# Performance work log

Hardware: AMD Instinct MI355X
Metric: run time of the kernel (lower is better)

Reference implementation:

```python
import jax, jax.numpy as jnp
import numpy as np
from jax import lax

N_NODES = 19
N_FILT = 8
CONV_CH = N_NODES * N_FILT  # 152
T = 512
POOL = 4
T_POOL = T // POOL  # 128
GCN_OUT = 16
FLAT = N_NODES * GCN_OUT * T_POOL  # 38912
HID = 128
N_CLS = 2
BN_EPS = 1e-5


def setup_inputs() -> dict:
    key = jax.random.key(0)
    ks = jax.random.split(key, 12)
    B = 1024
    x = jax.random.normal(ks[0], (B, N_NODES, T), dtype=jnp.float32)
    # grouped Conv1d(19 -> 152, k=5, groups=19): kernel (out_ch, in_ch/groups=1, k)
    conv_w = jax.random.normal(ks[1], (CONV_CH, 1, 5), dtype=jnp.float32) * 0.2
    conv_b = jax.random.normal(ks[2], (CONV_CH,), dtype=jnp.float32) * 0.05
    bn_gamma = jnp.ones((CONV_CH,), jnp.float32)
    bn_beta = jnp.zeros((CONV_CH,), jnp.float32)
    bn_mean = jax.random.normal(ks[3], (CONV_CH,), dtype=jnp.float32) * 0.1
    bn_var = jax.random.uniform(ks[4], (CONV_CH,), dtype=jnp.float32, minval=0.5, maxval=1.5)
    adj = jax.random.uniform(ks[5], (N_NODES, N_NODES), dtype=jnp.float32)
    gcn_w = jax.random.normal(ks[6], (GCN_OUT, N_FILT), dtype=jnp.float32) * (1.0 / np.sqrt(N_FILT))
    gcn_b = jnp.zeros((GCN_OUT,), jnp.float32)
    w1 = jax.random.normal(ks[7], (HID, FLAT), dtype=jnp.float32) * (1.0 / np.sqrt(FLAT))
    b1 = jnp.zeros((HID,), jnp.float32)
    w2 = jax.random.normal(ks[8], (N_CLS, HID), dtype=jnp.float32) * (1.0 / np.sqrt(HID))
    b2 = jnp.zeros((N_CLS,), jnp.float32)
    return dict(x=x, conv_w=conv_w, conv_b=conv_b, bn_gamma=bn_gamma, bn_beta=bn_beta,
                bn_mean=bn_mean, bn_var=bn_var, adj=adj, gcn_w=gcn_w, gcn_b=gcn_b,
                w1=w1, b1=b1, w2=w2, b2=b2)


def reference(x, conv_w, conv_b, bn_gamma, bn_beta, bn_mean, bn_var, adj,
              gcn_w, gcn_b, w1, b1, w2, b2):
    B = x.shape[0]
    # depthwise temporal conv: [B,19,T] -> [B,152,T]
    h = lax.conv_general_dilated(x, conv_w, window_strides=(1,), padding=[(2, 2)],
                                 feature_group_count=N_NODES,
                                 dimension_numbers=('NCW', 'OIW', 'NCW'))
    h = h + conv_b[None, :, None]
    # BatchNorm1d (eval mode: running stats) + ReLU, fused elementwise
    inv = bn_gamma / jnp.sqrt(bn_var + BN_EPS)
    h = jax.nn.relu(h * inv[None, :, None] + (bn_beta - bn_mean * inv)[None, :, None])
    # MaxPool1d(4): [B,152,512] -> [B,152,128]
    h = h.reshape(B, CONV_CH, T_POOL, POOL).max(axis=-1)
    # view -> [B,19,8,128]
    h = h.reshape(B, N_NODES, N_FILT, T_POOL)
    # softmax adjacency aggregation: bift = A_ij * bjft
    A = jax.nn.softmax(adj, axis=1)
    support = jnp.einsum('ij,bjft->bift', A, h)
    # permute to [B,19,128,8], linear 8->16, ReLU
    g = jax.nn.relu(jnp.einsum('bnft,of->bnto', support, gcn_w) + gcn_b)
    # classifier: flatten -> Linear(38912,128) -> ReLU -> (Dropout eval=identity) -> Linear(128,2)
    flat = g.reshape(B, FLAT)
    hid = jax.nn.relu(flat @ w1.T + b1)
    return hid @ w2.T + b2
```

## Files before the change

### kernel.cpp

```cpp
#include <hip/hip_runtime.h>

#define NB    1024
#define NN    19
#define NF    8
#define CCH   152
#define TLEN  512
#define TP    128
#define GO    16
#define KFLAT 38912
#define HID   128
#define NCLS  2
#define NROWS (NB*TP)
#define KC    152
#define KP    160
#define NJP   20
#define NOUT  304
#define M2R   320

#define KTILE 1024
#define NKT   (KFLAT / KTILE)

typedef float  f32x4  __attribute__((ext_vector_type(4)));
typedef __bf16 bf16x8 __attribute__((ext_vector_type(8)));
typedef __bf16 bf16x4 __attribute__((ext_vector_type(4)));
typedef unsigned short u16x8 __attribute__((ext_vector_type(8)));

__device__ __forceinline__ void gload16(const __bf16* g, __bf16* l) {
    __builtin_amdgcn_global_load_lds(
        (const __attribute__((address_space(1))) void*)g,
        (__attribute__((address_space(3))) void*)l, 16, 0, 0);
}

__global__ __launch_bounds__(256) void prep_small(
    const float* __restrict__ adj,
    const float* __restrict__ bn_gamma, const float* __restrict__ bn_beta,
    const float* __restrict__ bn_mean,  const float* __restrict__ bn_var,
    const float* __restrict__ conv_b,
    float* __restrict__ A_g, float* __restrict__ bnS, float* __restrict__ bnB)
{
    const int tid = threadIdx.x;
    if (tid < NN) {
        float v[NN];
        float m = -1e30f;
        #pragma unroll
        for (int j = 0; j < NN; ++j) { v[j] = adj[tid * NN + j]; m = fmaxf(m, v[j]); }
        float s = 0.f;
        #pragma unroll
        for (int j = 0; j < NN; ++j) { v[j] = expf(v[j] - m); s += v[j]; }
        float rc = 1.f / s;
        #pragma unroll
        for (int j = 0; j < NN; ++j) A_g[tid * NN + j] = v[j] * rc;
    }
    if (tid >= 64 && tid < 64 + CCH) {
        int c = tid - 64;
        float inv = bn_gamma[c] * rsqrtf(bn_var[c] + 1e-5f);
        bnS[c] = inv;
        bnB[c] = conv_b[c] * inv + bn_beta[c] - bn_mean[c] * inv;
    }
}

__global__ __launch_bounds__(256) void prep_m2(
    const float* __restrict__ A_g, const float* __restrict__ gcn_w,
    __bf16* __restrict__ m2g)
{
    int i = blockIdx.x * 256 + threadIdx.x;
    if (i >= M2R * KP) return;
    int c = i / KP, k = i - c * KP;
    float v = 0.f;
    if (c < NOUT && k < KC) {
        int n = c >> 4, o = c & 15;
        int j = k >> 3, f = k & 7;
        v = A_g[n * NN + j] * gcn_w[o * NF + f];
    }
    m2g[i] = (__bf16)v;
}

__global__ __launch_bounds__(128) void conv_pool(
    const float* __restrict__ x,
    const float* __restrict__ conv_w,
    const float* __restrict__ bnS, const float* __restrict__ bnB,
    __bf16* __restrict__ H)
{
    const int bid = blockIdx.x;
    const int b = bid / NN, n = bid - b * NN;
    const int tp = threadIdx.x;

    const float* xr = x + ((size_t)b * NN + n) * TLEN;
    const float4 f4z = {0.f, 0.f, 0.f, 0.f};
    float4 L0 = (tp > 0)   ? *(const float4*)(xr + 4 * tp - 4) : f4z;
    float4 L1 =              *(const float4*)(xr + 4 * tp);
    float4 L2 = (tp < 127) ? *(const float4*)(xr + 4 * tp + 4) : f4z;
    float xv[9] = {L0.z, L0.w, L1.x, L1.y, L1.z, L1.w, L2.x, L2.y, L2.z};

    const float* cw = conv_w + n * (NF * 5);
    const float* Sp = bnS + n * NF;
    const float* Bp = bnB + n * NF;

    union { __bf16 h[8]; u16x8 v; } hv;
    #pragma unroll
    for (int f = 0; f < NF; ++f) {
        float w0 = cw[f*5+0], w1 = cw[f*5+1], w2 = cw[f*5+2], w3 = cw[f*5+3], w4 = cw[f*5+4];
        float s = Sp[f], bb = Bp[f];
        float m = -1e30f;
        #pragma unroll
        for (int p = 0; p < 4; ++p) {
            float a = xv[p]*w0 + xv[p+1]*w1 + xv[p+2]*w2 + xv[p+3]*w3 + xv[p+4]*w4;
            m = fmaxf(m, a * s + bb);
        }
        hv.h[f] = (__bf16)fmaxf(m, 0.f);
    }
    size_t row = (size_t)b * TP + tp;
    *(u16x8*)(H + ((size_t)n * NROWS + row) * 8) = hv.v;
    if (n == NN - 1) {
        u16x8 z = {0,0,0,0,0,0,0,0};
        *(u16x8*)(H + ((size_t)(NJP - 1) * NROWS + row) * 8) = z;
    }
}

__global__ __launch_bounds__(640) void mix_gcn(
    const __bf16* __restrict__ H,
    const __bf16* __restrict__ m2g,
    const float* __restrict__ gcn_b,
    __bf16* __restrict__ g2)
{
    const int tid  = threadIdx.x;
    const int lane = tid & 63, w = tid >> 6;
    const int arow = lane & 15;
    const int jg   = lane >> 4;
    const int ct0  = w * 2;

    const float4 gbv = *(const float4*)(gcn_b + jg * 4);

    bf16x8 mf[2][5];
    #pragma unroll
    for (int ct = 0; ct < 2; ++ct)
        #pragma unroll
        for (int ks = 0; ks < 5; ++ks)
            mf[ct][ks] = *(const bf16x8*)(
                m2g + (size_t)((ct0 + ct) * 16 + arow) * KP + ks * 32 + jg * 8);

    const int b = blockIdx.x;
    const __bf16* hbase = H + (size_t)arow * 8 + (size_t)jg * (NROWS * 8);

    bf16x8 afb[2][5];
    #pragma unroll
    for (int ks = 0; ks < 5; ++ks)
        afb[0][ks] = *(const bf16x8*)(hbase + ((size_t)b * TP) * 8 + (size_t)ks * 4 * (NROWS * 8));

    #pragma unroll
    for (int it = 0; it < 8; ++it) {
        if (it + 1 < 8) {
            #pragma unroll
            for (int ks = 0; ks < 5; ++ks)
                afb[(it + 1) & 1][ks] = *(const bf16x8*)(
                    hbase + ((size_t)b * TP + (it + 1) * 16) * 8 + (size_t)ks * 4 * (NROWS * 8));
        }

        f32x4 acc[2];
        #pragma unroll
        for (int ct = 0; ct < 2; ++ct) acc[ct] = (f32x4){0.f, 0.f, 0.f, 0.f};

        #pragma unroll
        for (int ks = 0; ks < 5; ++ks)
            #pragma unroll
            for (int ct = 0; ct < 2; ++ct)
                acc[ct] = __builtin_amdgcn_mfma_f32_16x16x32_bf16(mf[ct][ks], afb[it & 1][ks], acc[ct], 0, 0, 0);

        const int t = it * 16 + arow;
        __bf16* gb2 = g2 + (size_t)b * KFLAT + t * 16 + jg * 4;
        #pragma unroll
        for (int ct = 0; ct < 2; ++ct) {
            const int n = ct0 + ct;
            if (n < NN) {
                bf16x4 v;
                v[0] = (__bf16)fmaxf(acc[ct][0] + gbv.x, 0.f);
                v[1] = (__bf16)fmaxf(acc[ct][1] + gbv.y, 0.f);
                v[2] = (__bf16)fmaxf(acc[ct][2] + gbv.z, 0.f);
                v[3] = (__bf16)fmaxf(acc[ct][3] + gbv.w, 0.f);
                *(bf16x4*)(gb2 + n * (TP * GO)) = v;
            }
        }
    }
}

__global__ __launch_bounds__(256) void w1_to_bf16(
    const float* __restrict__ w1, __bf16* __restrict__ o)
{
    const int n4 = (HID * KFLAT) >> 2;
    for (int i = blockIdx.x * 256 + threadIdx.x; i < n4; i += gridDim.x * 256) {
        float4 v = ((const float4*)w1)[i];
        bf16x4 r;
        r[0] = (__bf16)v.x; r[1] = (__bf16)v.y; r[2] = (__bf16)v.z; r[3] = (__bf16)v.w;
        ((bf16x4*)o)[i] = r;
    }
}

__global__ __launch_bounds__(256) void gemm_fc1(
    const __bf16* __restrict__ gmat,
    const __bf16* __restrict__ wmat,
    float* __restrict__ partial)
{
    __shared__ __align__(16) __bf16 At[128][32];
    __shared__ __align__(16) __bf16 Bt[128][32];

    const int tid = threadIdx.x;
    const int b0 = blockIdx.x * 128;
    const int k0 = blockIdx.y * KTILE;

    const int lane = tid & 63;
    const int w = tid >> 6;
    const int wm = (w >> 1) * 64;
    const int wn = (w & 1) * 64;

    const int srow_off = lane >> 2;
    const int schunk   = ((lane & 3) ^ (srow_off & 3)) * 8;

    f32x4 acc[4][4];
    #pragma unroll
    for (int m = 0; m < 4; ++m)
        #pragma unroll
        for (int n = 0; n < 4; ++n) acc[m][n] = (f32x4){0.f, 0.f, 0.f, 0.f};

    const int arow = lane & 15;
    const int rsw  = ((lane >> 4) ^ (arow & 3)) * 8;

    for (int ks = 0; ks < KTILE / 32; ++ks) {
        const int gk = k0 + ks * 32;
        const int r0 = w * 16;
        const int r1 = 64 + w * 16;
        gload16(gmat + (size_t)(b0 + r0 + srow_off) * KFLAT + gk + schunk, &At[r0][0]);
        gload16(gmat + (size_t)(b0 + r1 + srow_off) * KFLAT + gk + schunk, &At[r1][0]);
        gload16(wmat + (size_t)(r0 + srow_off) * KFLAT + gk + schunk, &Bt[r0][0]);
        gload16(wmat + (size_t)(r1 + srow_off) * KFLAT + gk + schunk, &Bt[r1][0]);
        __syncthreads();

        bf16x8 af[4], bfr[4];
        #pragma unroll
        for (int m = 0; m < 4; ++m) af[m]  = *(const bf16x8*)(&At[0][0] + (wm + m * 16 + arow) * 32 + rsw);
        #pragma unroll
        for (int n = 0; n < 4; ++n) bfr[n] = *(const bf16x8*)(&Bt[0][0] + (wn + n * 16 + arow) * 32 + rsw);
        #pragma unroll
        for (int m = 0; m < 4; ++m)
            #pragma unroll
            for (int n = 0; n < 4; ++n)
                acc[m][n] = __builtin_amdgcn_mfma_f32_16x16x32_bf16(af[m], bfr[n], acc[m][n], 0, 0, 0);
        __syncthreads();
    }

    float* pout = partial + (size_t)blockIdx.y * (NB * HID);
    #pragma unroll
    for (int m = 0; m < 4; ++m) {
        const int rbase = b0 + wm + m * 16 + (lane >> 4) * 4;
        #pragma unroll
        for (int n = 0; n < 4; ++n) {
            const int col = wn + n * 16 + (lane & 15);
            #pragma unroll
            for (int r = 0; r < 4; ++r)
                pout[(size_t)(rbase + r) * HID + col] = acc[m][n][r];
        }
    }
}

__global__ __launch_bounds__(128) void reduce_fc2(
    const float* __restrict__ partial,
    const float* __restrict__ b1,
    const float* __restrict__ w2,
    const float* __restrict__ b2,
    float* __restrict__ out)
{
    __shared__ float red0[128], red1[128];
    const int b = blockIdx.x, j = threadIdx.x;
    float s = b1[j];
    #pragma unroll 2
    for (int p = 0; p < NKT; ++p) s += partial[(size_t)p * (NB * HID) + b * HID + j];
    float h = fmaxf(s, 0.f);
    red0[j] = h * w2[j];
    red1[j] = h * w2[HID + j];
    __syncthreads();
    for (int off = 64; off > 0; off >>= 1) {
        if (j < off) { red0[j] += red0[j + off]; red1[j] += red1[j + off]; }
        __syncthreads();
    }
    if (j == 0) {
        out[b * 2 + 0] = red0[0] + b2[0];
        out[b * 2 + 1] = red1[0] + b2[1];
    }
}

extern "C" void kernel_launch(void* const* d_in, const int* in_sizes, int n_in,
                              void* d_out, int out_size, void* d_ws, size_t ws_size,
                              hipStream_t stream) {
    const float* x        = (const float*)d_in[0];
    const float* conv_w   = (const float*)d_in[1];
    const float* conv_b   = (const float*)d_in[2];
    const float* bn_gamma = (const float*)d_in[3];
    const float* bn_beta  = (const float*)d_in[4];
    const float* bn_mean  = (const float*)d_in[5];
    const float* bn_var   = (const float*)d_in[6];
    const float* adj      = (const float*)d_in[7];
    const float* gcn_w    = (const float*)d_in[8];
    const float* gcn_b    = (const float*)d_in[9];
    const float* w1       = (const float*)d_in[10];
    const float* b1       = (const float*)d_in[11];
    const float* w2       = (const float*)d_in[12];
    const float* b2       = (const float*)d_in[13];
    float* out = (float*)d_out;

    char* ws = (char*)d_ws;
    __bf16* g2   = (__bf16*)ws;
    __bf16* Hbuf = (__bf16*)(ws + 79691776);
    __bf16* w1b  = (__bf16*)(ws + 79691776);
    float*  part = (float*)(ws + 89653248);
    __bf16* m2g  = (__bf16*)(ws + 121634816);
    float*  A_g  = (float*)(ws + 121737216);
    float*  bnS  = (float*)(ws + 121739264);
    float*  bnB  = (float*)(ws + 121740288);

    prep_small<<<dim3(1), dim3(256), 0, stream>>>(
        adj, bn_gamma, bn_beta, bn_mean, bn_var, conv_b, A_g, bnS, bnB);
    prep_m2<<<dim3(200), dim3(256), 0, stream>>>(A_g, gcn_w, m2g);
    conv_pool<<<dim3(NB * NN), dim3(128), 0, stream>>>(x, conv_w, bnS, bnB, Hbuf);
    mix_gcn<<<dim3(NB), dim3(640), 0, stream>>>(Hbuf, m2g, gcn_b, g2);
    w1_to_bf16<<<dim3(1024), dim3(256), 0, stream>>>(w1, w1b);
    gemm_fc1<<<dim3(8, NKT), dim3(256), 0, stream>>>(g2, w1b, part);
    reduce_fc2<<<dim3(NB), dim3(128), 0, stream>>>(part, b1, w2, b2, out);
}
```

Baseline: 108.5 us.

## Merge prep kernels, fold w1 bf16 conversion into conv launch, retile FC1 split-K

```diff
diff --git a/kernel.cpp b/kernel.cpp
--- a/kernel.cpp
+++ b/kernel.cpp
@@ -17,8 +17,11 @@
 #define NOUT  304
 #define M2R   320
 
-#define KTILE 1024
+#define KTILE 608
 #define NKT   (KFLAT / KTILE)
+
+#define W1N4    ((HID * KFLAT) / 4)
+#define W1BLKS  2048
 
 typedef float  f32x4  __attribute__((ext_vector_type(4)));
 typedef __bf16 bf16x8 __attribute__((ext_vector_type(8)));
@@ -31,13 +34,15 @@
         (__attribute__((address_space(3))) void*)l, 16, 0, 0);
 }
 
-__global__ __launch_bounds__(256) void prep_small(
+__global__ __launch_bounds__(256) void prep(
     const float* __restrict__ adj,
     const float* __restrict__ bn_gamma, const float* __restrict__ bn_beta,
     const float* __restrict__ bn_mean,  const float* __restrict__ bn_var,
-    const float* __restrict__ conv_b,
-    float* __restrict__ A_g, float* __restrict__ bnS, float* __restrict__ bnB)
-{
+    const float* __restrict__ conv_b,   const float* __restrict__ gcn_w,
+    float* __restrict__ bnS, float* __restrict__ bnB,
+    __bf16* __restrict__ m2g)
+{
+    __shared__ float As[NN * NN];
     const int tid = threadIdx.x;
     if (tid < NN) {
         float v[NN];
@@ -49,7 +54,7 @@
         for (int j = 0; j < NN; ++j) { v[j] = expf(v[j] - m); s += v[j]; }
         float rc = 1.f / s;
         #pragma unroll
-        for (int j = 0; j < NN; ++j) A_g[tid * NN + j] = v[j] * rc;
+        for (int j = 0; j < NN; ++j) As[tid * NN + j] = v[j] * rc;
     }
     if (tid >= 64 && tid < 64 + CCH) {
         int c = tid - 64;
@@ -57,31 +62,36 @@
         bnS[c] = inv;
         bnB[c] = conv_b[c] * inv + bn_beta[c] - bn_mean[c] * inv;
     }
-}
-
-__global__ __launch_bounds__(256) void prep_m2(
-    const float* __restrict__ A_g, const float* __restrict__ gcn_w,
-    __bf16* __restrict__ m2g)
-{
-    int i = blockIdx.x * 256 + threadIdx.x;
-    if (i >= M2R * KP) return;
-    int c = i / KP, k = i - c * KP;
-    float v = 0.f;
-    if (c < NOUT && k < KC) {
-        int n = c >> 4, o = c & 15;
-        int j = k >> 3, f = k & 7;
-        v = A_g[n * NN + j] * gcn_w[o * NF + f];
-    }
-    m2g[i] = (__bf16)v;
-}
-
-__global__ __launch_bounds__(128) void conv_pool(
+    __syncthreads();
+    for (int i = tid; i < M2R * KP; i += 256) {
+        int c = i / KP, k = i - c * KP;
+        float v = 0.f;
+        if (c < NOUT && k < KC) {
+            int n = c >> 4, o = c & 15;
+            int j = k >> 3, f = k & 7;
+            v = As[n * NN + j] * gcn_w[o * NF + f];
+        }
+        m2g[i] = (__bf16)v;
+    }
+}
+
+__global__ __launch_bounds__(128) void conv_w1(
     const float* __restrict__ x,
     const float* __restrict__ conv_w,
     const float* __restrict__ bnS, const float* __restrict__ bnB,
-    __bf16* __restrict__ H)
+    __bf16* __restrict__ H,
+    const float* __restrict__ w1, __bf16* __restrict__ w1b)
 {
     const int bid = blockIdx.x;
+    if (bid >= NB * NN) {
+        for (int i = (bid - NB * NN) * 128 + threadIdx.x; i < W1N4; i += W1BLKS * 128) {
+            float4 v = ((const float4*)w1)[i];
+            bf16x4 r;
+            r[0] = (__bf16)v.x; r[1] = (__bf16)v.y; r[2] = (__bf16)v.z; r[3] = (__bf16)v.w;
+            ((bf16x4*)w1b)[i] = r;
+        }
+        return;
+    }
     const int b = bid / NN, n = bid - b * NN;
     const int tp = threadIdx.x;
 
@@ -99,12 +109,12 @@
     union { __bf16 h[8]; u16x8 v; } hv;
     #pragma unroll
     for (int f = 0; f < NF; ++f) {
-        float w0 = cw[f*5+0], w1 = cw[f*5+1], w2 = cw[f*5+2], w3 = cw[f*5+3], w4 = cw[f*5+4];
+        float w0 = cw[f*5+0], w1v = cw[f*5+1], w2 = cw[f*5+2], w3 = cw[f*5+3], w4 = cw[f*5+4];
         float s = Sp[f], bb = Bp[f];
         float m = -1e30f;
         #pragma unroll
         for (int p = 0; p < 4; ++p) {
-            float a = xv[p]*w0 + xv[p+1]*w1 + xv[p+2]*w2 + xv[p+3]*w3 + xv[p+4]*w4;
+            float a = xv[p]*w0 + xv[p+1]*w1v + xv[p+2]*w2 + xv[p+3]*w3 + xv[p+4]*w4;
             m = fmaxf(m, a * s + bb);
         }
         hv.h[f] = (__bf16)fmaxf(m, 0.f);
@@ -183,18 +193,6 @@
     }
 }
 
-__global__ __launch_bounds__(256) void w1_to_bf16(
-    const float* __restrict__ w1, __bf16* __restrict__ o)
-{
-    const int n4 = (HID * KFLAT) >> 2;
-    for (int i = blockIdx.x * 256 + threadIdx.x; i < n4; i += gridDim.x * 256) {
-        float4 v = ((const float4*)w1)[i];
-        bf16x4 r;
-        r[0] = (__bf16)v.x; r[1] = (__bf16)v.y; r[2] = (__bf16)v.z; r[3] = (__bf16)v.w;
-        ((bf16x4*)o)[i] = r;
-    }
-}
-
 __global__ __launch_bounds__(256) void gemm_fc1(
     const __bf16* __restrict__ gmat,
     const __bf16* __restrict__ wmat,
@@ -204,8 +202,9 @@
     __shared__ __align__(16) __bf16 Bt[128][32];
 
     const int tid = threadIdx.x;
-    const int b0 = blockIdx.x * 128;
-    const int k0 = blockIdx.y * KTILE;
+    const int kt = blockIdx.x;
+    const int b0 = blockIdx.y * 128;
+    const int k0 = kt * KTILE;
 
     const int lane = tid & 63;
     const int w = tid >> 6;
@@ -247,7 +246,7 @@
         __syncthreads();
     }
 
-    float* pout = partial + (size_t)blockIdx.y * (NB * HID);
+    float* pout = partial + (size_t)kt * (NB * HID);
     #pragma unroll
     for (int m = 0; m < 4; ++m) {
         const int rbase = b0 + wm + m * 16 + (lane >> 4) * 4;
@@ -271,7 +270,7 @@
     __shared__ float red0[128], red1[128];
     const int b = blockIdx.x, j = threadIdx.x;
     float s = b1[j];
-    #pragma unroll 2
+    #pragma unroll 4
     for (int p = 0; p < NKT; ++p) s += partial[(size_t)p * (NB * HID) + b * HID + j];
     float h = fmaxf(s, 0.f);
     red0[j] = h * w2[j];
@@ -309,19 +308,17 @@
     char* ws = (char*)d_ws;
     __bf16* g2   = (__bf16*)ws;
     __bf16* Hbuf = (__bf16*)(ws + 79691776);
-    __bf16* w1b  = (__bf16*)(ws + 79691776);
-    float*  part = (float*)(ws + 89653248);
-    __bf16* m2g  = (__bf16*)(ws + 121634816);
-    float*  A_g  = (float*)(ws + 121737216);
-    float*  bnS  = (float*)(ws + 121739264);
-    float*  bnB  = (float*)(ws + 121740288);
-
-    prep_small<<<dim3(1), dim3(256), 0, stream>>>(
-        adj, bn_gamma, bn_beta, bn_mean, bn_var, conv_b, A_g, bnS, bnB);
-    prep_m2<<<dim3(200), dim3(256), 0, stream>>>(A_g, gcn_w, m2g);
-    conv_pool<<<dim3(NB * NN), dim3(128), 0, stream>>>(x, conv_w, bnS, bnB, Hbuf);
+    __bf16* w1b  = (__bf16*)(ws + 121634816);
+    float*  part = (float*)(ws + 131596288);
+    __bf16* m2g  = (__bf16*)(ws + 165150720);
+    float*  bnS  = (float*)(ws + 165253120);
+    float*  bnB  = (float*)(ws + 165255168);
+
+    prep<<<dim3(1), dim3(256), 0, stream>>>(
+        adj, bn_gamma, bn_beta, bn_mean, bn_var, conv_b, gcn_w, bnS, bnB, m2g);
+    conv_w1<<<dim3(NB * NN + W1BLKS), dim3(128), 0, stream>>>(
+        x, conv_w, bnS, bnB, Hbuf, w1, w1b);
     mix_gcn<<<dim3(NB), dim3(640), 0, stream>>>(Hbuf, m2g, gcn_b, g2);
-    w1_to_bf16<<<dim3(1024), dim3(256), 0, stream>>>(w1, w1b);
-    gemm_fc1<<<dim3(8, NKT), dim3(256), 0, stream>>>(g2, w1b, part);
+    gemm_fc1<<<dim3(NKT, 8), dim3(256), 0, stream>>>(g2, w1b, part);
     reduce_fc2<<<dim3(NB), dim3(128), 0, stream>>>(part, b1, w2, b2, out);
 }
```

Result: slower. 118.2 us (+9.0%).
